# Optimization experiments

Measured on AMD Instinct MI355X. Metric: run time of the kernel, lower is better.

## Reference

```python
import jax, jax.numpy as jnp
import numpy as np

H = W = 240

def setup_inputs() -> dict:
    key = jax.random.key(0)
    k1, k2, k3 = jax.random.split(key, 3)
    B = 256
    T2_Gen = jax.random.normal(k1, (B, 1, H, W), dtype=jnp.float32)
    underT2_K = jax.random.normal(k2, (B, 2, H, W), dtype=jnp.float32)
    # k-space sampling mask (soft in [0,1); original uses a fixed undersampling mask)
    A = jax.random.uniform(k3, (H, W), dtype=jnp.float32)
    return {"T2_Gen": T2_Gen, "underT2_K": underT2_K, "A": A}

def reference(T2_Gen, underT2_K, A):
    # x2: [B, H, W]
    x2 = T2_Gen.reshape(-1, H, W)
    # batched 2D FFT over the last two axes (replaces the per-slice numpy loop)
    x2_k = jnp.fft.fft2(x2)  # complex64
    # undersampled k-space as complex: real = channel 0, imag = channel 1
    y_k = underT2_K[:, 0, :, :] + 1j * underT2_K[:, 1, :, :]
    z_k = (1.0 - A) * x2_k + y_k
    z = jnp.abs(jnp.fft.ifft2(z_k))  # [B, H, W] real
    return z.reshape(-1, 1, H, W)
```

## Files before the change

### kernel.cpp

```cpp
#include <hip/hip_runtime.h>
#include <hip/hip_fp16.h>
#include <math.h>

#define HW 240
#define PITCH 241
#define IMG_PIX (HW*HW)
#define NB 15
#define TILE_ELEMS (240*16)

__device__ __forceinline__ float2 cmul(float2 a, float2 b){
    return make_float2(a.x*b.x - a.y*b.y, a.x*b.y + a.y*b.x);
}
__device__ __forceinline__ float2 cadd(float2 a, float2 b){
    return make_float2(a.x+b.x, a.y+b.y);
}
__device__ __forceinline__ float2 csub(float2 a, float2 b){
    return make_float2(a.x-b.x, a.y-b.y);
}
__device__ __forceinline__ __half2 f2h(float2 a){ return __floats2half2_rn(a.x, a.y); }
__device__ __forceinline__ float2 h2f(__half2 h){ return make_float2(__low2float(h), __high2float(h)); }

template<int SIGN>
__device__ __forceinline__ void dft15(const float2* x, float2* X){
    const float S = (float)SIGN;
    const float s3 = 0.8660254037844387f;
    float2 y[5][3];
    #pragma unroll
    for (int n2 = 0; n2 < 5; ++n2){
        float2 a0 = x[n2], a1 = x[5+n2], a2 = x[10+n2];
        float2 t = cadd(a1, a2);
        float2 u = csub(a1, a2);
        float2 m = make_float2(a0.x - 0.5f*t.x, a0.y - 0.5f*t.y);
        float sx = S * s3;
        float2 s = make_float2(-sx*u.y, sx*u.x);
        y[n2][0] = cadd(a0, t);
        y[n2][1] = cadd(m, s);
        y[n2][2] = csub(m, s);
    }
    const float C15[9] = {1.f, 0.9135454576426009f, 0.6691306063588582f, 0.30901699437494745f,
                          -0.10452846326765346f, -0.5f, -0.8090169943749475f,
                          -0.9781476007338057f, -0.9781476007338057f};
    const float S15[9] = {0.f, 0.4067366430758004f, 0.7431448254773942f, 0.9510565162951535f,
                          0.9945218953682733f, 0.8660254037844387f, 0.5877852522924731f,
                          0.20791169081775931f, -0.20791169081775931f};
    #pragma unroll
    for (int n2 = 1; n2 < 5; ++n2){
        #pragma unroll
        for (int k1 = 1; k1 < 3; ++k1){
            const int e = n2*k1;
            y[n2][k1] = cmul(y[n2][k1], make_float2(C15[e], S*S15[e]));
        }
    }
    const float c1 = 0.30901699437494745f, s1 = 0.9510565162951535f;
    const float c2 = -0.8090169943749475f, s2 = 0.5877852522924731f;
    #pragma unroll
    for (int k1 = 0; k1 < 3; ++k1){
        float2 x0 = y[0][k1], x1 = y[1][k1], x2 = y[2][k1], x3 = y[3][k1], x4 = y[4][k1];
        float2 t1 = cadd(x1, x4), t3 = csub(x1, x4);
        float2 t2 = cadd(x2, x3), t4 = csub(x2, x3);
        X[k1] = make_float2(x0.x + t1.x + t2.x, x0.y + t1.y + t2.y);
        float2 u1 = make_float2(x0.x + c1*t1.x + c2*t2.x, x0.y + c1*t1.y + c2*t2.y);
        float2 u2 = make_float2(x0.x + c2*t1.x + c1*t2.x, x0.y + c2*t1.y + c1*t2.y);
        float2 v1 = make_float2(S*(s1*t3.x + s2*t4.x), S*(s1*t3.y + s2*t4.y));
        float2 v2 = make_float2(S*(s2*t3.x - s1*t4.x), S*(s2*t3.y - s1*t4.y));
        X[k1+3]  = make_float2(u1.x - v1.y, u1.y + v1.x);
        X[k1+12] = make_float2(u1.x + v1.y, u1.y - v1.x);
        X[k1+6]  = make_float2(u2.x - v2.y, u2.y + v2.x);
        X[k1+9]  = make_float2(u2.x + v2.y, u2.y - v2.x);
    }
}

template<int SIGN>
__device__ __forceinline__ void dft16(const float2* x, float2* X){
    const float S = (float)SIGN;
    float2 y[4][4];
    #pragma unroll
    for (int n2 = 0; n2 < 4; ++n2){
        float2 a0 = x[n2], a1 = x[4+n2], a2 = x[8+n2], a3 = x[12+n2];
        float2 t0 = cadd(a0,a2), t1 = csub(a0,a2);
        float2 t2 = cadd(a1,a3), t3 = csub(a1,a3);
        float2 it3 = make_float2(-S*t3.y, S*t3.x);
        y[n2][0] = cadd(t0,t2);
        y[n2][2] = csub(t0,t2);
        y[n2][1] = cadd(t1,it3);
        y[n2][3] = csub(t1,it3);
    }
    const float C16[10] = {1.f, 0.9238795325112867f, 0.7071067811865476f, 0.3826834323650898f,
                           0.f, -0.3826834323650898f, -0.7071067811865476f, -0.9238795325112867f,
                           -1.f, -0.9238795325112867f};
    const float S16[10] = {0.f, 0.3826834323650898f, 0.7071067811865476f, 0.9238795325112867f,
                           1.f, 0.9238795325112867f, 0.7071067811865476f, 0.3826834323650898f,
                           0.f, -0.3826834323650898f};
    #pragma unroll
    for (int n2 = 1; n2 < 4; ++n2){
        #pragma unroll
        for (int k1 = 1; k1 < 4; ++k1){
            const int e = n2*k1;
            y[n2][k1] = cmul(y[n2][k1], make_float2(C16[e], S*S16[e]));
        }
    }
    #pragma unroll
    for (int k1 = 0; k1 < 4; ++k1){
        float2 a0 = y[0][k1], a1 = y[1][k1], a2 = y[2][k1], a3 = y[3][k1];
        float2 t0 = cadd(a0,a2), t1 = csub(a0,a2);
        float2 t2 = cadd(a1,a3), t3 = csub(a1,a3);
        float2 it3 = make_float2(-S*t3.y, S*t3.x);
        X[k1]    = cadd(t0,t2);
        X[k1+8]  = csub(t0,t2);
        X[k1+4]  = cadd(t1,it3);
        X[k1+12] = csub(t1,it3);
    }
}

template<int SIGN>
__device__ void fft240(float2 (*sm)[PITCH], float2* v, int rl, int b){
    const float TWOPI = 6.28318530717958647692f;
    float2 Y[15];
    dft15<SIGN>(v, Y);
    float2 step, tw = make_float2(1.0f, 0.0f);
    {
        float ang = (float)SIGN * TWOPI * (float)b * (1.0f/240.0f);
        __sincosf(ang, &step.y, &step.x);
    }
    #pragma unroll
    for (int d = 0; d < 15; ++d){
        sm[rl][b*15 + d] = cmul(Y[d], tw);
        tw = cmul(tw, step);
    }
    __syncthreads();

    float2 Z[16];
    if (b < 15){
        #pragma unroll
        for (int bb = 0; bb < 16; ++bb) Z[bb] = sm[rl][bb*15 + b];
    }
    __syncthreads();
    if (b < 15){
        float2 XX[16];
        dft16<SIGN>(Z, XX);
        #pragma unroll
        for (int m = 0; m < 16; ++m) sm[rl][15*m + b] = XX[m];
    }
    __syncthreads();
}

__global__ __launch_bounds__(256) void passA_rowfft(const float* __restrict__ x,
                                                    __half2* __restrict__ out){
    __shared__ float2 sm[16][PITCH];
    float* smf = (float*)sm;
    int g = blockIdx.x, img = g / NB, h0 = (g % NB) * 16;
    int tid = threadIdx.x, rl = tid >> 4, b = tid & 15;
    const float* src = x + (size_t)img * IMG_PIX + (size_t)h0 * HW;
    #pragma unroll
    for (int j = 0; j < 15; ++j){
        int f = j*256 + tid;
        smf[(f/HW)*(2*PITCH) + (f%HW)] = src[f];
    }
    __syncthreads();
    float2 v[15];
    #pragma unroll
    for (int a = 0; a < 15; ++a) v[a] = make_float2(smf[rl*(2*PITCH) + 16*a + b], 0.0f);
    __syncthreads();
    fft240<-1>(sm, v, rl, b);
    int hl = rl, kwin = b;
    #pragma unroll
    for (int kb = 0; kb < NB; ++kb){
        float2 val = sm[hl][kb*16 + kwin];
        out[((size_t)(img*NB + kb)*HW + h0 + hl)*16 + kwin] = f2h(val);
    }
}

__global__ __launch_bounds__(256) void passB_col_dc_icol(__half2* __restrict__ io,
                                                         const float* __restrict__ under,
                                                         const float* __restrict__ Am){
    __shared__ float2 sm[16][PITCH];
    int g = blockIdx.x, img = g / NB, s = g % NB, kw0 = s * 16;
    int tid = threadIdx.x, rl = tid >> 4, b = tid & 15;
    __half2* chunk = io + (size_t)(img*NB + s) * TILE_ELEMS;
    #pragma unroll
    for (int j = 0; j < 15; ++j){
        int f = j*256 + tid;
        sm[f & 15][f >> 4] = h2f(chunk[f]);
    }
    __syncthreads();
    float2 v[15];
    #pragma unroll
    for (int a = 0; a < 15; ++a) v[a] = sm[rl][16*a + b];
    __syncthreads();
    fft240<-1>(sm, v, rl, b);

    const float* y0 = under + (size_t)img * (2*IMG_PIX);
    const float* y1 = y0 + IMG_PIX;
    #pragma unroll
    for (int j = 0; j < 15; ++j){
        int kh = j*16 + rl;
        size_t p = (size_t)kh * HW + kw0 + b;
        float sc = 1.0f - Am[p];
        float2 X = sm[b][kh];
        sm[b][kh] = make_float2(sc * X.x + y0[p], sc * X.y + y1[p]);
    }
    __syncthreads();
    #pragma unroll
    for (int a = 0; a < 15; ++a) v[a] = sm[rl][16*a + b];
    __syncthreads();
    fft240<+1>(sm, v, rl, b);

    const float inv240 = 1.0f / 240.0f;
    #pragma unroll
    for (int j = 0; j < 15; ++j){
        int f = j*256 + tid;
        float2 val = sm[f & 15][f >> 4];
        val.x *= inv240; val.y *= inv240;
        chunk[f] = f2h(val);
    }
}

__global__ __launch_bounds__(256) void passC_irow_abs(const __half2* __restrict__ in,
                                                      float* __restrict__ outp){
    __shared__ float2 sm[16][PITCH];
    int g = blockIdx.x, img = g / NB, h0 = (g % NB) * 16;
    int tid = threadIdx.x, rl = tid >> 4, b = tid & 15;
    int hl = rl, kwin = b;
    #pragma unroll
    for (int kb = 0; kb < NB; ++kb){
        __half2 hv = in[((size_t)(img*NB + kb)*HW + h0 + hl)*16 + kwin];
        sm[hl][kb*16 + kwin] = h2f(hv);
    }
    __syncthreads();
    float2 v[15];
    #pragma unroll
    for (int a = 0; a < 15; ++a) v[a] = sm[rl][16*a + b];
    __syncthreads();
    fft240<+1>(sm, v, rl, b);
    float* dst = outp + (size_t)img * IMG_PIX + (size_t)h0 * HW;
    const float inv240 = 1.0f / 240.0f;
    #pragma unroll
    for (int j = 0; j < 15; ++j){
        int f = j*256 + tid;
        float2 X = sm[f/HW][f%HW];
        dst[f] = sqrtf(X.x*X.x + X.y*X.y) * inv240;
    }
}

extern "C" void kernel_launch(void* const* d_in, const int* in_sizes, int n_in,
                              void* d_out, int out_size, void* d_ws, size_t ws_size,
                              hipStream_t stream){
    const float* T2   = (const float*)d_in[0];
    const float* U    = (const float*)d_in[1];
    const float* Am   = (const float*)d_in[2];
    float* out        = (float*)d_out;

    const int B = 256;
    __half2* i1 = (__half2*)d_ws;

    dim3 grid(B * NB), block(256);
    passA_rowfft     <<<grid, block, 0, stream>>>(T2, i1);
    passB_col_dc_icol<<<grid, block, 0, stream>>>(i1, U, Am);
    passC_irow_abs   <<<grid, block, 0, stream>>>(i1, out);
}
```

Baseline: 280.1 us.

## Replace block barriers with wave barriers in row FFTs and vectorize global I/O

Each row of the tile is handled by 16 lanes inside one 64-wide wavefront, so the block-wide __syncthreads inside fft240 and around the register loads become wave-level barriers. Block barriers are kept only where data crosses rows. Global loads and stores in all three passes are widened to float4 using 240 threads, and the shared pitch is padded to 242 for 16-byte alignment. This cuts barrier stalls and memory instruction count, but correctness now depends on each row's threads sharing a wavefront, and the new pitch may change LDS bank conflicts.

```diff
diff --git a/kernel.cpp b/kernel.cpp
--- a/kernel.cpp
+++ b/kernel.cpp
@@ -3,7 +3,8 @@
 #include <math.h>
 
 #define HW 240
-#define PITCH 241
+#define PITCH 242
+#define SMF_PITCH (2*PITCH)
 #define IMG_PIX (HW*HW)
 #define NB 15
 #define TILE_ELEMS (240*16)
@@ -19,6 +20,8 @@
 }
 __device__ __forceinline__ __half2 f2h(float2 a){ return __floats2half2_rn(a.x, a.y); }
 __device__ __forceinline__ float2 h2f(__half2 h){ return make_float2(__low2float(h), __high2float(h)); }
+
+__device__ __forceinline__ void wave_fence(){ __builtin_amdgcn_wave_barrier(); }
 
 template<int SIGN>
 __device__ __forceinline__ void dft15(const float2* x, float2* X){
@@ -127,67 +130,77 @@
         sm[rl][b*15 + d] = cmul(Y[d], tw);
         tw = cmul(tw, step);
     }
-    __syncthreads();
-
+    wave_fence();
     float2 Z[16];
     if (b < 15){
         #pragma unroll
         for (int bb = 0; bb < 16; ++bb) Z[bb] = sm[rl][bb*15 + b];
     }
-    __syncthreads();
+    wave_fence();
     if (b < 15){
         float2 XX[16];
         dft16<SIGN>(Z, XX);
         #pragma unroll
         for (int m = 0; m < 16; ++m) sm[rl][15*m + b] = XX[m];
     }
-    __syncthreads();
+    wave_fence();
 }
 
 __global__ __launch_bounds__(256) void passA_rowfft(const float* __restrict__ x,
                                                     __half2* __restrict__ out){
-    __shared__ float2 sm[16][PITCH];
+    __shared__ __align__(16) float2 sm[16][PITCH];
     float* smf = (float*)sm;
     int g = blockIdx.x, img = g / NB, h0 = (g % NB) * 16;
     int tid = threadIdx.x, rl = tid >> 4, b = tid & 15;
     const float* src = x + (size_t)img * IMG_PIX + (size_t)h0 * HW;
-    #pragma unroll
-    for (int j = 0; j < 15; ++j){
-        int f = j*256 + tid;
-        smf[(f/HW)*(2*PITCH) + (f%HW)] = src[f];
+    if (tid < 240){
+        #pragma unroll
+        for (int jj = 0; jj < 4; ++jj){
+            int k = jj*240 + tid;
+            int r = k / 60, c = 4*(k - r*60);
+            float4 d = *(const float4*)(src + 4*k);
+            *(float4*)(smf + r*SMF_PITCH + c) = d;
+        }
     }
     __syncthreads();
     float2 v[15];
     #pragma unroll
-    for (int a = 0; a < 15; ++a) v[a] = make_float2(smf[rl*(2*PITCH) + 16*a + b], 0.0f);
-    __syncthreads();
+    for (int a = 0; a < 15; ++a) v[a] = make_float2(smf[rl*SMF_PITCH + 16*a + b], 0.0f);
+    wave_fence();
     fft240<-1>(sm, v, rl, b);
-    int hl = rl, kwin = b;
     #pragma unroll
     for (int kb = 0; kb < NB; ++kb){
-        float2 val = sm[hl][kb*16 + kwin];
-        out[((size_t)(img*NB + kb)*HW + h0 + hl)*16 + kwin] = f2h(val);
+        float2 val = sm[rl][kb*16 + b];
+        out[((size_t)(img*NB + kb)*HW + h0 + rl)*16 + b] = f2h(val);
     }
 }
 
 __global__ __launch_bounds__(256) void passB_col_dc_icol(__half2* __restrict__ io,
                                                          const float* __restrict__ under,
                                                          const float* __restrict__ Am){
-    __shared__ float2 sm[16][PITCH];
+    __shared__ __align__(16) float2 sm[16][PITCH];
     int g = blockIdx.x, img = g / NB, s = g % NB, kw0 = s * 16;
     int tid = threadIdx.x, rl = tid >> 4, b = tid & 15;
     __half2* chunk = io + (size_t)(img*NB + s) * TILE_ELEMS;
-    #pragma unroll
-    for (int j = 0; j < 15; ++j){
-        int f = j*256 + tid;
-        sm[f & 15][f >> 4] = h2f(chunk[f]);
+    if (tid < 240){
+        #pragma unroll
+        for (int jj = 0; jj < 4; ++jj){
+            int k = jj*240 + tid;
+            float4 raw = *(const float4*)(chunk + 4*k);
+            const __half2* hp = (const __half2*)&raw;
+            int col = k >> 2;
+            int r0 = (4*k) & 15;
+            #pragma unroll
+            for (int i = 0; i < 4; ++i) sm[r0 + i][col] = h2f(hp[i]);
+        }
     }
     __syncthreads();
     float2 v[15];
     #pragma unroll
     for (int a = 0; a < 15; ++a) v[a] = sm[rl][16*a + b];
-    __syncthreads();
+    wave_fence();
     fft240<-1>(sm, v, rl, b);
+    __syncthreads();
 
     const float* y0 = under + (size_t)img * (2*IMG_PIX);
     const float* y1 = y0 + IMG_PIX;
@@ -202,43 +215,61 @@
     __syncthreads();
     #pragma unroll
     for (int a = 0; a < 15; ++a) v[a] = sm[rl][16*a + b];
-    __syncthreads();
+    wave_fence();
     fft240<+1>(sm, v, rl, b);
+    __syncthreads();
 
     const float inv240 = 1.0f / 240.0f;
-    #pragma unroll
-    for (int j = 0; j < 15; ++j){
-        int f = j*256 + tid;
-        float2 val = sm[f & 15][f >> 4];
-        val.x *= inv240; val.y *= inv240;
-        chunk[f] = f2h(val);
+    if (tid < 240){
+        #pragma unroll
+        for (int jj = 0; jj < 4; ++jj){
+            int k = jj*240 + tid;
+            int col = k >> 2;
+            int r0 = (4*k) & 15;
+            float4 outv;
+            __half2* op = (__half2*)&outv;
+            #pragma unroll
+            for (int i = 0; i < 4; ++i){
+                float2 val = sm[r0 + i][col];
+                op[i] = f2h(make_float2(val.x*inv240, val.y*inv240));
+            }
+            *(float4*)(chunk + 4*k) = outv;
+        }
     }
 }
 
 __global__ __launch_bounds__(256) void passC_irow_abs(const __half2* __restrict__ in,
                                                       float* __restrict__ outp){
-    __shared__ float2 sm[16][PITCH];
+    __shared__ __align__(16) float2 sm[16][PITCH];
     int g = blockIdx.x, img = g / NB, h0 = (g % NB) * 16;
     int tid = threadIdx.x, rl = tid >> 4, b = tid & 15;
-    int hl = rl, kwin = b;
     #pragma unroll
     for (int kb = 0; kb < NB; ++kb){
-        __half2 hv = in[((size_t)(img*NB + kb)*HW + h0 + hl)*16 + kwin];
-        sm[hl][kb*16 + kwin] = h2f(hv);
-    }
-    __syncthreads();
+        __half2 hv = in[((size_t)(img*NB + kb)*HW + h0 + rl)*16 + b];
+        sm[rl][kb*16 + b] = h2f(hv);
+    }
+    wave_fence();
     float2 v[15];
     #pragma unroll
     for (int a = 0; a < 15; ++a) v[a] = sm[rl][16*a + b];
-    __syncthreads();
+    wave_fence();
     fft240<+1>(sm, v, rl, b);
+    __syncthreads();
     float* dst = outp + (size_t)img * IMG_PIX + (size_t)h0 * HW;
     const float inv240 = 1.0f / 240.0f;
-    #pragma unroll
-    for (int j = 0; j < 15; ++j){
-        int f = j*256 + tid;
-        float2 X = sm[f/HW][f%HW];
-        dst[f] = sqrtf(X.x*X.x + X.y*X.y) * inv240;
+    if (tid < 240){
+        #pragma unroll
+        for (int jj = 0; jj < 4; ++jj){
+            int k = jj*240 + tid;
+            int r = k / 60, c = 4*(k - r*60);
+            float4 o;
+            float2 X0 = sm[r][c+0], X1 = sm[r][c+1], X2 = sm[r][c+2], X3 = sm[r][c+3];
+            o.x = sqrtf(X0.x*X0.x + X0.y*X0.y) * inv240;
+            o.y = sqrtf(X1.x*X1.x + X1.y*X1.y) * inv240;
+            o.z = sqrtf(X2.x*X2.x + X2.y*X2.y) * inv240;
+            o.w = sqrtf(X3.x*X3.x + X3.y*X3.y) * inv240;
+            *(float4*)(dst + 4*k) = o;
+        }
     }
 }
 
```

After: 274.2 us. 2.1% less time.

## Pack two real rows per complex FFT, use wave barriers, load and store directly

Applied to the files above, without the earlier changes.

Pass A now packs two real input rows into one complex FFT and separates them with the conjugate-symmetry split, halving the row-FFT work and the block count. The block-wide __syncthreads calls are replaced with wave-level barriers, which relies on each 16-thread FFT row group staying inside one wavefront. The shared-memory staging loops for global loads and stores are removed, so registers are filled from and written to global memory directly. The data-consistency step is fused into the registers right after the forward column FFT, and PITCH changes to 242. Direct strided global access may coalesce less well than the staged copies.

```diff
diff --git a/kernel.cpp b/kernel.cpp
--- a/kernel.cpp
+++ b/kernel.cpp
@@ -3,9 +3,10 @@
 #include <math.h>
 
 #define HW 240
-#define PITCH 241
+#define PITCH 242
 #define IMG_PIX (HW*HW)
 #define NB 15
+#define NBA 8
 #define TILE_ELEMS (240*16)
 
 __device__ __forceinline__ float2 cmul(float2 a, float2 b){
@@ -19,6 +20,8 @@
 }
 __device__ __forceinline__ __half2 f2h(float2 a){ return __floats2half2_rn(a.x, a.y); }
 __device__ __forceinline__ float2 h2f(__half2 h){ return make_float2(__low2float(h), __high2float(h)); }
+
+__device__ __forceinline__ void wave_fence(){ __builtin_amdgcn_wave_barrier(); }
 
 template<int SIGN>
 __device__ __forceinline__ void dft15(const float2* x, float2* X){
@@ -113,8 +116,10 @@
 }
 
 template<int SIGN>
-__device__ void fft240(float2 (*sm)[PITCH], float2* v, int rl, int b){
+__device__ __forceinline__ void fft240_core(float2 (*sm)[PITCH], float2* v,
+                                            float2* XX, int rl, int b){
     const float TWOPI = 6.28318530717958647692f;
+    wave_fence();
     float2 Y[15];
     dft15<SIGN>(v, Y);
     float2 step, tw = make_float2(1.0f, 0.0f);
@@ -127,118 +132,117 @@
         sm[rl][b*15 + d] = cmul(Y[d], tw);
         tw = cmul(tw, step);
     }
-    __syncthreads();
-
+    wave_fence();
     float2 Z[16];
     if (b < 15){
         #pragma unroll
         for (int bb = 0; bb < 16; ++bb) Z[bb] = sm[rl][bb*15 + b];
     }
-    __syncthreads();
-    if (b < 15){
-        float2 XX[16];
-        dft16<SIGN>(Z, XX);
+    wave_fence();
+    if (b < 15) dft16<SIGN>(Z, XX);
+}
+
+template<int SIGN>
+__device__ __forceinline__ void fft240(float2 (*sm)[PITCH], float2* v, int rl, int b){
+    float2 XX[16];
+    fft240_core<SIGN>(sm, v, XX, rl, b);
+    if (b < 15){
         #pragma unroll
         for (int m = 0; m < 16; ++m) sm[rl][15*m + b] = XX[m];
     }
-    __syncthreads();
+    wave_fence();
 }
 
 __global__ __launch_bounds__(256) void passA_rowfft(const float* __restrict__ x,
                                                     __half2* __restrict__ out){
-    __shared__ float2 sm[16][PITCH];
-    float* smf = (float*)sm;
-    int g = blockIdx.x, img = g / NB, h0 = (g % NB) * 16;
+    __shared__ __align__(16) float2 sm[15][PITCH];
+    int g = blockIdx.x, img = g / NBA, h0 = (g % NBA) * 30;
     int tid = threadIdx.x, rl = tid >> 4, b = tid & 15;
-    const float* src = x + (size_t)img * IMG_PIX + (size_t)h0 * HW;
-    #pragma unroll
-    for (int j = 0; j < 15; ++j){
-        int f = j*256 + tid;
-        smf[(f/HW)*(2*PITCH) + (f%HW)] = src[f];
-    }
-    __syncthreads();
+    if (tid >= 240) return;
+    const float* r0 = x + (size_t)img * IMG_PIX + (size_t)(h0 + 2*rl) * HW;
+    const float* r1 = r0 + HW;
     float2 v[15];
     #pragma unroll
-    for (int a = 0; a < 15; ++a) v[a] = make_float2(smf[rl*(2*PITCH) + 16*a + b], 0.0f);
-    __syncthreads();
+    for (int a = 0; a < 15; ++a)
+        v[a] = make_float2(r0[16*a + b], r1[16*a + b]);
     fft240<-1>(sm, v, rl, b);
-    int hl = rl, kwin = b;
     #pragma unroll
     for (int kb = 0; kb < NB; ++kb){
-        float2 val = sm[hl][kb*16 + kwin];
-        out[((size_t)(img*NB + kb)*HW + h0 + hl)*16 + kwin] = f2h(val);
+        int k = kb*16 + b;
+        int km = k ? 240 - k : 0;
+        float2 P = sm[rl][k], Q = sm[rl][km];
+        float2 Xa = make_float2(0.5f*(P.x + Q.x), 0.5f*(P.y - Q.y));
+        float2 Xb = make_float2(0.5f*(P.y + Q.y), 0.5f*(Q.x - P.x));
+        size_t o = ((size_t)(img*NB + kb)*HW + (h0 + 2*rl))*16 + b;
+        out[o]      = f2h(Xa);
+        out[o + 16] = f2h(Xb);
     }
 }
 
 __global__ __launch_bounds__(256) void passB_col_dc_icol(__half2* __restrict__ io,
                                                          const float* __restrict__ under,
                                                          const float* __restrict__ Am){
-    __shared__ float2 sm[16][PITCH];
+    __shared__ __align__(16) float2 sm[16][PITCH];
     int g = blockIdx.x, img = g / NB, s = g % NB, kw0 = s * 16;
     int tid = threadIdx.x, rl = tid >> 4, b = tid & 15;
     __half2* chunk = io + (size_t)(img*NB + s) * TILE_ELEMS;
-    #pragma unroll
-    for (int j = 0; j < 15; ++j){
-        int f = j*256 + tid;
-        sm[f & 15][f >> 4] = h2f(chunk[f]);
-    }
-    __syncthreads();
+
     float2 v[15];
     #pragma unroll
-    for (int a = 0; a < 15; ++a) v[a] = sm[rl][16*a + b];
-    __syncthreads();
-    fft240<-1>(sm, v, rl, b);
-
-    const float* y0 = under + (size_t)img * (2*IMG_PIX);
-    const float* y1 = y0 + IMG_PIX;
-    #pragma unroll
-    for (int j = 0; j < 15; ++j){
-        int kh = j*16 + rl;
-        size_t p = (size_t)kh * HW + kw0 + b;
-        float sc = 1.0f - Am[p];
-        float2 X = sm[b][kh];
-        sm[b][kh] = make_float2(sc * X.x + y0[p], sc * X.y + y1[p]);
-    }
-    __syncthreads();
-    #pragma unroll
-    for (int a = 0; a < 15; ++a) v[a] = sm[rl][16*a + b];
-    __syncthreads();
-    fft240<+1>(sm, v, rl, b);
+    for (int a = 0; a < 15; ++a)
+        v[a] = h2f(chunk[(size_t)(16*a + b)*16 + rl]);
+
+    float2 XX[16];
+    fft240_core<-1>(sm, v, XX, rl, b);
+
+    if (b < 15){
+        const float* y0 = under + (size_t)img * (2*IMG_PIX);
+        const float* y1 = y0 + IMG_PIX;
+        #pragma unroll
+        for (int m = 0; m < 16; ++m){
+            size_t p = (size_t)(15*m + b) * HW + kw0 + rl;
+            float sc = 1.0f - Am[p];
+            XX[m] = make_float2(sc * XX[m].x + y0[p], sc * XX[m].y + y1[p]);
+        }
+        #pragma unroll
+        for (int m = 0; m < 16; ++m) sm[rl][15*m + b] = XX[m];
+    }
+    wave_fence();
+
+    float2 v2[15];
+    #pragma unroll
+    for (int a = 0; a < 15; ++a) v2[a] = sm[rl][16*a + b];
+    float2 ZZ[16];
+    fft240_core<+1>(sm, v2, ZZ, rl, b);
 
     const float inv240 = 1.0f / 240.0f;
-    #pragma unroll
-    for (int j = 0; j < 15; ++j){
-        int f = j*256 + tid;
-        float2 val = sm[f & 15][f >> 4];
-        val.x *= inv240; val.y *= inv240;
-        chunk[f] = f2h(val);
+    if (b < 15){
+        #pragma unroll
+        for (int m = 0; m < 16; ++m)
+            chunk[(size_t)(15*m + b)*16 + rl] =
+                f2h(make_float2(ZZ[m].x*inv240, ZZ[m].y*inv240));
     }
 }
 
 __global__ __launch_bounds__(256) void passC_irow_abs(const __half2* __restrict__ in,
                                                       float* __restrict__ outp){
-    __shared__ float2 sm[16][PITCH];
+    __shared__ __align__(16) float2 sm[16][PITCH];
     int g = blockIdx.x, img = g / NB, h0 = (g % NB) * 16;
     int tid = threadIdx.x, rl = tid >> 4, b = tid & 15;
-    int hl = rl, kwin = b;
-    #pragma unroll
-    for (int kb = 0; kb < NB; ++kb){
-        __half2 hv = in[((size_t)(img*NB + kb)*HW + h0 + hl)*16 + kwin];
-        sm[hl][kb*16 + kwin] = h2f(hv);
-    }
-    __syncthreads();
     float2 v[15];
     #pragma unroll
-    for (int a = 0; a < 15; ++a) v[a] = sm[rl][16*a + b];
-    __syncthreads();
-    fft240<+1>(sm, v, rl, b);
-    float* dst = outp + (size_t)img * IMG_PIX + (size_t)h0 * HW;
+    for (int a = 0; a < 15; ++a)
+        v[a] = h2f(in[((size_t)(img*NB + a)*HW + h0 + rl)*16 + b]);
+    float2 XX[16];
+    fft240_core<+1>(sm, v, XX, rl, b);
     const float inv240 = 1.0f / 240.0f;
-    #pragma unroll
-    for (int j = 0; j < 15; ++j){
-        int f = j*256 + tid;
-        float2 X = sm[f/HW][f%HW];
-        dst[f] = sqrtf(X.x*X.x + X.y*X.y) * inv240;
+    float* dst = outp + (size_t)img * IMG_PIX + (size_t)(h0 + rl) * HW;
+    if (b < 15){
+        #pragma unroll
+        for (int m = 0; m < 16; ++m){
+            float2 X = XX[m];
+            dst[15*m + b] = sqrtf(X.x*X.x + X.y*X.y) * inv240;
+        }
     }
 }
 
@@ -253,8 +257,8 @@
     const int B = 256;
     __half2* i1 = (__half2*)d_ws;
 
-    dim3 grid(B * NB), block(256);
-    passA_rowfft     <<<grid, block, 0, stream>>>(T2, i1);
-    passB_col_dc_icol<<<grid, block, 0, stream>>>(i1, U, Am);
-    passC_irow_abs   <<<grid, block, 0, stream>>>(i1, out);
-}
+    dim3 block(256);
+    passA_rowfft     <<<dim3(B * NBA), block, 0, stream>>>(T2, i1);
+    passB_col_dc_icol<<<dim3(B * NB),  block, 0, stream>>>(i1, U, Am);
+    passC_irow_abs   <<<dim3(B * NB),  block, 0, stream>>>(i1, out);
+}
```

Result: slower. 346.6 us (+23.7%).
